# Optimization experiments

Hardware: AMD Instinct MI355X
Metric: run time of the kernel (lower is better)

The kernel has to match this reference:

```python
import jax, jax.numpy as jnp
import numpy as np

B = 16384
D = 1024          # in_features
R = 64            # low_rank
E = 4             # num_experts
L = 3             # layer_num


def setup_inputs() -> dict:
    key = jax.random.key(0)
    ks = jax.random.split(key, 6)
    # xavier-normal-ish scales
    s_uv = (2.0 / (D + R)) ** 0.5
    s_c = (2.0 / (R + R)) ** 0.5
    s_g = (2.0 / (D + 1)) ** 0.5
    return {
        "inputs": jax.random.normal(ks[0], (B, D), dtype=jnp.float32),
        "U": jax.random.normal(ks[1], (L, E, D, R), dtype=jnp.float32) * s_uv,
        "V": jax.random.normal(ks[2], (L, E, D, R), dtype=jnp.float32) * s_uv,
        "C": jax.random.normal(ks[3], (L, E, R, R), dtype=jnp.float32) * s_c,
        "gate_w": jax.random.normal(ks[4], (E, D), dtype=jnp.float32) * s_g,
        "bias": jnp.zeros((L, D), dtype=jnp.float32),
    }


def reference(inputs, U, V, C, gate_w, bias):
    x0 = inputs                                  # [B, D]
    x_l = x0
    for i in range(L):
        # gating: per-expert Linear(d,1) on x_l -> [B, E], softmax over experts
        gates = jax.nn.softmax(x_l @ gate_w.T, axis=1)        # [B, E]
        # v_x = tanh(V_e^T x_l) for all experts at once
        v = jnp.tanh(jnp.einsum('bd,edr->ber', x_l, V[i]))    # [B, E, R]
        v = jnp.tanh(jnp.einsum('ers,bes->ber', C[i], v))     # [B, E, R]
        uv = jnp.einsum('edr,ber->bed', U[i], v)              # [B, E, D]
        dot = x0[:, None, :] * (uv + bias[i][None, None, :])  # [B, E, D]
        moe_out = jnp.einsum('bed,be->bd', dot, gates)        # [B, D]
        x_l = moe_out + x_l
    return x_l
```

## Files before the change

### kernel.cpp

```cpp
#include <hip/hip_runtime.h>
#include <math.h>

#define BB 16384
#define DD 1024
#define RR 64
#define EE 4
#define ER 256
#define LL 3

#define LDM 72

typedef __bf16 bf16x8 __attribute__((ext_vector_type(8)));
typedef float f32x4 __attribute__((ext_vector_type(4)));
typedef unsigned short us;

static __device__ inline us f2b(float f) {
    union { float f; unsigned u; } c; c.f = f;
    return (us)((c.u + 0x7FFF + ((c.u >> 16) & 1)) >> 16);
}
static __device__ inline float b2f(us v) {
    union { unsigned u; float f; } c; c.u = ((unsigned)v) << 16;
    return c.f;
}
static __device__ inline float fast_tanh(float x) {
    float t = __expf(2.f * x);
    return 1.f - 2.f / (t + 1.f);
}
static __device__ __forceinline__ void ld_lds16(const us* g, us* l) {
    __builtin_amdgcn_global_load_lds((const __attribute__((address_space(1))) void*)g,
                                     (__attribute__((address_space(3))) void*)l, 16, 0, 0);
}

__global__ __launch_bounds__(256) void convF2B(const float* __restrict__ s, us* __restrict__ d) {
    int f = (blockIdx.x * 256 + threadIdx.x) * 4;
    float4 v = *(const float4*)&s[f];
    *(ushort4*)&d[f] = make_ushort4(f2b(v.x), f2b(v.y), f2b(v.z), f2b(v.w));
}
__global__ __launch_bounds__(256) void convV(const float* __restrict__ V, us* __restrict__ Vt) {
    const int le = blockIdx.x;
    const int d0 = blockIdx.y * 64;
    __shared__ float t[64 * 65];
    const int tid = threadIdx.x;
    const float* Vb = V + (size_t)le * DD * RR;
    #pragma unroll
    for (int p = 0; p < 4; ++p) {
        int f = tid + p * 256; int dd = f >> 4; int c = (f & 15) * 4;
        float4 v = *(const float4*)&Vb[(size_t)(d0 + dd) * RR + c];
        t[dd * 65 + c + 0] = v.x; t[dd * 65 + c + 1] = v.y;
        t[dd * 65 + c + 2] = v.z; t[dd * 65 + c + 3] = v.w;
    }
    __syncthreads();
    int r = tid >> 2, dg = (tid & 3) * 16;
    us o[16];
    #pragma unroll
    for (int k = 0; k < 16; ++k) o[k] = f2b(t[(dg + k) * 65 + r]);
    us* dst = Vt + (size_t)le * RR * DD + (size_t)r * DD + d0 + dg;
    #pragma unroll
    for (int q = 0; q < 4; ++q) *(ushort4*)&dst[q * 4] = *(ushort4*)&o[q * 4];
}

__global__ __launch_bounds__(512, 2) void layer_fused(const us* __restrict__ xs,
                                                      const us* __restrict__ Vt,
                                                      const us* __restrict__ Ce,
                                                      const us* __restrict__ gwb,
                                                      const us* __restrict__ x0b,
                                                      const us* __restrict__ Ub,
                                                      us* __restrict__ xbo,
                                                      const float* __restrict__ biasl,
                                                      float* __restrict__ out, int last) {
    const int row0 = blockIdx.x * 64;
    const int tid = threadIdx.x;
    const int lane = tid & 63, wave = tid >> 6;
    const int l15 = lane & 15, quad = lane >> 4;
    const int e = wave & 3, h = wave >> 2;
    const int e64 = e * 64;

    __shared__ __align__(16) union {
        struct { us buf[4][10240]; us gw[4096]; float gates[256]; } s;
        us Tt[4][64 * LDM];
        struct { us wlds[64 * 256]; float smf[8][1024]; } p2;
    } u;

    const int kcA  = (lane & 3) ^ ((lane >> 3) & 3);
    const int sA   = quad ^ ((l15 >> 1) & 3);
    const int rsub = lane >> 2;

    ld_lds16(gwb + (size_t)(lane & 3) * DD + (wave * 16 + rsub) * 8, &u.s.gw[wave * 512]);

    auto STAGE = [&](int bi, int k0) {
        us* bb = u.s.buf[bi];
        #pragma unroll
        for (int j = 0; j < 2; ++j) {
            int row = wave * 32 + j * 16 + rsub;
            ld_lds16(Vt + (size_t)row * DD + k0 + kcA * 8, &bb[(wave * 32 + j * 16) * 32]);
        }
        if (wave < 4) {
            int row = wave * 16 + rsub;
            ld_lds16(xs + (size_t)(row0 + row) * DD + k0 + kcA * 8, &bb[8192 + wave * 512]);
        }
    };

    f32x4 acc[4][2] = {};
    f32x4 accg = {};
    STAGE(0, 0); STAGE(1, 32); STAGE(2, 64);

    for (int t = 0; t < 32; ++t) {
        if (t < 30) {
            if (wave < 4) asm volatile("s_waitcnt vmcnt(6)" ::: "memory");
            else          asm volatile("s_waitcnt vmcnt(4)" ::: "memory");
        } else if (t == 30) {
            if (wave < 4) asm volatile("s_waitcnt vmcnt(3)" ::: "memory");
            else          asm volatile("s_waitcnt vmcnt(2)" ::: "memory");
        } else {
            asm volatile("s_waitcnt vmcnt(0)" ::: "memory");
        }
        __builtin_amdgcn_s_barrier();
        if (t < 29) STAGE((t + 3) & 3, (t + 3) * 32);
        __builtin_amdgcn_sched_barrier(0);
        const us* bb = u.s.buf[t & 3];
        bf16x8 af[4], bfr[2];
        #pragma unroll
        for (int mt = 0; mt < 4; ++mt)
            af[mt] = *(const bf16x8*)&bb[(e64 + mt * 16 + l15) * 32 + sA * 8];
        #pragma unroll
        for (int nt = 0; nt < 2; ++nt)
            bfr[nt] = *(const bf16x8*)&bb[8192 + (h * 32 + nt * 16 + l15) * 32 + sA * 8];
        #pragma unroll
        for (int mt = 0; mt < 4; ++mt)
            #pragma unroll
            for (int nt = 0; nt < 2; ++nt)
                acc[mt][nt] = __builtin_amdgcn_mfma_f32_16x16x32_bf16(af[mt], bfr[nt], acc[mt][nt], 0, 0, 0);
        if (wave < 4) {
            bf16x8 bfrg = *(const bf16x8*)&bb[8192 + (wave * 16 + l15) * 32 + sA * 8];
            bf16x8 afg  = *(const bf16x8*)&u.s.gw[(t * 4 + quad) * 32 + (l15 & 3) * 8];
            accg = __builtin_amdgcn_mfma_f32_16x16x32_bf16(afg, bfrg, accg, 0, 0, 0);
        }
    }
    __builtin_amdgcn_s_barrier();
    __builtin_amdgcn_sched_barrier(0);

    {
        us* Tt = u.Tt[e];
        #pragma unroll
        for (int mt = 0; mt < 4; ++mt)
            #pragma unroll
            for (int nt = 0; nt < 2; ++nt) {
                int b = h * 32 + nt * 16 + l15;
                us o[4];
                #pragma unroll
                for (int i = 0; i < 4; ++i) o[i] = f2b(fast_tanh(acc[mt][nt][i]));
                *(ushort4*)&Tt[b * LDM + mt * 16 + quad * 4] = *(ushort4*)o;
            }
    }
    if (wave < 4 && quad == 0) {
        float l0 = accg[0], l1 = accg[1], l2 = accg[2], l3 = accg[3];
        float m = fmaxf(fmaxf(l0, l1), fmaxf(l2, l3));
        float g0 = __expf(l0 - m), g1 = __expf(l1 - m);
        float g2 = __expf(l2 - m), g3 = __expf(l3 - m);
        float inv = 1.f / (g0 + g1 + g2 + g3);
        int b = wave * 16 + l15;
        u.s.gates[0 * 64 + b] = g0 * inv; u.s.gates[1 * 64 + b] = g1 * inv;
        u.s.gates[2 * 64 + b] = g2 * inv; u.s.gates[3 * 64 + b] = g3 * inv;
    }
    __syncthreads();

    const us* Cb = Ce + (size_t)e * RR * RR;
    f32x4 acc2[4][2] = {};
    #pragma unroll
    for (int ks = 0; ks < 2; ++ks) {
        bf16x8 af2[4], bf2[2];
        #pragma unroll
        for (int mt = 0; mt < 4; ++mt)
            af2[mt] = *(const bf16x8*)&Cb[(size_t)(mt * 16 + l15) * RR + ks * 32 + quad * 8];
        #pragma unroll
        for (int nt = 0; nt < 2; ++nt)
            bf2[nt] = *(const bf16x8*)&u.Tt[e][(h * 32 + nt * 16 + l15) * LDM + ks * 32 + quad * 8];
        #pragma unroll
        for (int mt = 0; mt < 4; ++mt)
            #pragma unroll
            for (int nt = 0; nt < 2; ++nt)
                acc2[mt][nt] = __builtin_amdgcn_mfma_f32_16x16x32_bf16(af2[mt], bf2[nt], acc2[mt][nt], 0, 0, 0);
    }
    __syncthreads();

    #pragma unroll
    for (int mt = 0; mt < 4; ++mt)
        #pragma unroll
        for (int nt = 0; nt < 2; ++nt) {
            int b = h * 32 + nt * 16 + l15;
            float g = u.s.gates[e64 + b];
            us o[4];
            #pragma unroll
            for (int i = 0; i < 4; ++i) o[i] = f2b(g * fast_tanh(acc2[mt][nt][i]));
            int col = e64 + mt * 16 + quad * 4;
            int cc = col >> 3, off = col & 7;
            *(ushort4*)&u.p2.wlds[b * 256 + ((cc ^ (b & 7)) << 3) + off] = *(ushort4*)o;
        }
    __syncthreads();

    const int bl = lane >> 2, dc3 = lane & 3;
    #pragma unroll 1
    for (int p = 0; p < 2; ++p) {
        const int dw = p * 512 + wave * 64;
        f32x4 pac[4][4] = {};
        #pragma unroll
        for (int s = 0; s < 8; ++s) {
            int e2 = s >> 1, r0 = (s & 1) * 32;
            bf16x8 af[4], bfr[4];
            #pragma unroll
            for (int mt = 0; mt < 4; ++mt) {
                int d = dw + mt * 16 + l15;
                af[mt] = *(const bf16x8*)&Ub[((size_t)e2 * DD + d) * RR + r0 + quad * 8];
            }
            #pragma unroll
            for (int nt = 0; nt < 4; ++nt) {
                int b = nt * 16 + l15;
                int cc = e2 * 8 + (r0 >> 3) + quad;
                bfr[nt] = *(const bf16x8*)&u.p2.wlds[b * 256 + ((cc ^ (b & 7)) << 3)];
            }
            #pragma unroll
            for (int mt = 0; mt < 4; ++mt)
                #pragma unroll
                for (int nt = 0; nt < 4; ++nt)
                    pac[mt][nt] = __builtin_amdgcn_mfma_f32_16x16x32_bf16(af[mt], bfr[nt], pac[mt][nt], 0, 0, 0);
        }
        const int dg = dw + dc3 * 16;
        float bfv[16];
        *(float4*)&bfv[0]  = *(const float4*)&biasl[dg];
        *(float4*)&bfv[4]  = *(const float4*)&biasl[dg + 4];
        *(float4*)&bfv[8]  = *(const float4*)&biasl[dg + 8];
        *(float4*)&bfv[12] = *(const float4*)&biasl[dg + 12];
        float* smf = u.p2.smf[wave];
        #pragma unroll
        for (int nt = 0; nt < 4; ++nt) {
            #pragma unroll
            for (int mt = 0; mt < 4; ++mt) {
                int ch = (mt * 4 + quad) ^ (l15 & 7);
                *(f32x4*)&smf[l15 * 64 + ch * 4] = pac[mt][nt];
            }
            asm volatile("s_waitcnt lgkmcnt(0)" ::: "memory");
            __builtin_amdgcn_sched_barrier(0);
            const int brow = row0 + nt * 16 + bl;
            const size_t gb = (size_t)brow * DD + dg;
            uint xu[8], lu[8];
            *(uint4*)&xu[0] = *(const uint4*)&x0b[gb];
            *(uint4*)&xu[4] = *(const uint4*)&x0b[gb + 8];
            *(uint4*)&lu[0] = *(const uint4*)&xs[gb];
            *(uint4*)&lu[4] = *(const uint4*)&xs[gb + 8];
            float o[16];
            #pragma unroll
            for (int j = 0; j < 4; ++j) {
                int ch = (dc3 * 4 + j) ^ (bl & 7);
                float4 a = *(const float4*)&smf[bl * 64 + ch * 4];
                #pragma unroll
                for (int i = 0; i < 4; ++i) {
                    int k = j * 4 + i;
                    float av = (i == 0) ? a.x : (i == 1) ? a.y : (i == 2) ? a.z : a.w;
                    uint uu = xu[k >> 1], ll = lu[k >> 1];
                    float xv = b2f((k & 1) ? (us)(uu >> 16) : (us)(uu & 0xffff));
                    float xl = b2f((k & 1) ? (us)(ll >> 16) : (us)(ll & 0xffff));
                    o[k] = xv * (av + bfv[k]) + xl;
                }
            }
            if (last) {
                *(float4*)&out[gb]      = *(float4*)&o[0];
                *(float4*)&out[gb + 4]  = *(float4*)&o[4];
                *(float4*)&out[gb + 8]  = *(float4*)&o[8];
                *(float4*)&out[gb + 12] = *(float4*)&o[12];
            } else {
                us ob[16];
                #pragma unroll
                for (int k = 0; k < 16; ++k) ob[k] = f2b(o[k]);
                *(uint4*)&xbo[gb]     = *(uint4*)&ob[0];
                *(uint4*)&xbo[gb + 8] = *(uint4*)&ob[8];
            }
            asm volatile("s_waitcnt lgkmcnt(0)" ::: "memory");
            __builtin_amdgcn_sched_barrier(0);
        }
    }
}

extern "C" void kernel_launch(void* const* d_in, const int* in_sizes, int n_in,
                              void* d_out, int out_size, void* d_ws, size_t ws_size,
                              hipStream_t stream) {
    const float* inputs = (const float*)d_in[0];
    const float* U      = (const float*)d_in[1];
    const float* V      = (const float*)d_in[2];
    const float* C      = (const float*)d_in[3];
    const float* gw     = (const float*)d_in[4];
    const float* bias   = (const float*)d_in[5];
    float* out = (float*)d_out;

    us* xb0 = (us*)d_ws;
    us* xb  = xb0 + (size_t)BB * DD;
    us* gwb = xb + (size_t)BB * DD;
    us* Vt  = gwb + (size_t)EE * DD;
    us* Ub  = Vt + (size_t)LL * EE * RR * DD;
    us* Cb  = Ub + (size_t)LL * EE * DD * RR;

    convF2B<<<dim3(BB * DD / 1024), 256, 0, stream>>>(inputs, xb0);
    convF2B<<<dim3(LL * EE * DD * RR / 1024), 256, 0, stream>>>(U, Ub);
    convF2B<<<dim3(LL * EE * RR * RR / 1024), 256, 0, stream>>>(C, Cb);
    convF2B<<<dim3(EE * DD / 1024), 256, 0, stream>>>(gw, gwb);
    convV<<<dim3(LL * EE, DD / 64), 256, 0, stream>>>(V, Vt);

    for (int i = 0; i < LL; ++i) {
        const us* xs = (i == 0) ? xb0 : xb;
        layer_fused<<<dim3(BB / 64), 512, 0, stream>>>(
            xs, Vt + (size_t)i * EE * RR * DD, Cb + (size_t)i * EE * RR * RR, gwb,
            xb0, Ub + (size_t)i * EE * DD * RR, xb, bias + (size_t)i * DD,
            out, i == LL - 1);
    }
}
```

Before: 278.7 us.

## Halve row tile to 32 and use triple buffering to raise occupancy

Each block now handles 32 batch rows instead of 64, doubling the grid, and launch bounds ask for 4 blocks per CU instead of 2. The staging pipeline drops from four LDS buffers to three with a prefetch distance of two, and LDS and accumulator sizes shrink to match. The goal is more resident waves to hide memory latency. In exchange, every block still streams the full V and U weight matrices for only half as many rows, so weight traffic and reuse per loaded byte get worse, and the shorter prefetch distance hides less latency per block.

```diff
diff --git a/kernel.cpp b/kernel.cpp
--- a/kernel.cpp
+++ b/kernel.cpp
@@ -59,7 +59,7 @@
     for (int q = 0; q < 4; ++q) *(ushort4*)&dst[q * 4] = *(ushort4*)&o[q * 4];
 }
 
-__global__ __launch_bounds__(512, 2) void layer_fused(const us* __restrict__ xs,
+__global__ __launch_bounds__(512, 4) void layer_fused(const us* __restrict__ xs,
                                                       const us* __restrict__ Vt,
                                                       const us* __restrict__ Ce,
                                                       const us* __restrict__ gwb,
@@ -68,7 +68,7 @@
                                                       us* __restrict__ xbo,
                                                       const float* __restrict__ biasl,
                                                       float* __restrict__ out, int last) {
-    const int row0 = blockIdx.x * 64;
+    const int row0 = blockIdx.x * 32;
     const int tid = threadIdx.x;
     const int lane = tid & 63, wave = tid >> 6;
     const int l15 = lane & 15, quad = lane >> 4;
@@ -76,9 +76,9 @@
     const int e64 = e * 64;
 
     __shared__ __align__(16) union {
-        struct { us buf[4][10240]; us gw[4096]; float gates[256]; } s;
-        us Tt[4][64 * LDM];
-        struct { us wlds[64 * 256]; float smf[8][1024]; } p2;
+        struct { us buf[3][9216]; us gw[4096]; float gates[128]; } s;
+        us Tt[4][32 * LDM];
+        struct { us wlds[32 * 256]; float smf[8][1024]; } p2;
     } u;
 
     const int kcA  = (lane & 3) ^ ((lane >> 3) & 3);
@@ -94,47 +94,45 @@
             int row = wave * 32 + j * 16 + rsub;
             ld_lds16(Vt + (size_t)row * DD + k0 + kcA * 8, &bb[(wave * 32 + j * 16) * 32]);
         }
-        if (wave < 4) {
+        if (wave < 2) {
             int row = wave * 16 + rsub;
             ld_lds16(xs + (size_t)(row0 + row) * DD + k0 + kcA * 8, &bb[8192 + wave * 512]);
         }
     };
 
-    f32x4 acc[4][2] = {};
+    f32x4 acc[4] = {};
     f32x4 accg = {};
-    STAGE(0, 0); STAGE(1, 32); STAGE(2, 64);
-
+    STAGE(0, 0); STAGE(1, 32);
+
+    int cur = 0;
     for (int t = 0; t < 32; ++t) {
-        if (t < 30) {
-            if (wave < 4) asm volatile("s_waitcnt vmcnt(6)" ::: "memory");
-            else          asm volatile("s_waitcnt vmcnt(4)" ::: "memory");
-        } else if (t == 30) {
-            if (wave < 4) asm volatile("s_waitcnt vmcnt(3)" ::: "memory");
+        if (t < 31) {
+            if (wave < 2) asm volatile("s_waitcnt vmcnt(3)" ::: "memory");
             else          asm volatile("s_waitcnt vmcnt(2)" ::: "memory");
         } else {
             asm volatile("s_waitcnt vmcnt(0)" ::: "memory");
         }
         __builtin_amdgcn_s_barrier();
-        if (t < 29) STAGE((t + 3) & 3, (t + 3) * 32);
+        if (t < 30) {
+            int st = cur + 2; if (st >= 3) st -= 3;
+            STAGE(st, (t + 2) * 32);
+        }
         __builtin_amdgcn_sched_barrier(0);
-        const us* bb = u.s.buf[t & 3];
-        bf16x8 af[4], bfr[2];
+        const us* bb = u.s.buf[cur];
+        bf16x8 af[4], bfr;
         #pragma unroll
         for (int mt = 0; mt < 4; ++mt)
             af[mt] = *(const bf16x8*)&bb[(e64 + mt * 16 + l15) * 32 + sA * 8];
-        #pragma unroll
-        for (int nt = 0; nt < 2; ++nt)
-            bfr[nt] = *(const bf16x8*)&bb[8192 + (h * 32 + nt * 16 + l15) * 32 + sA * 8];
+        bfr = *(const bf16x8*)&bb[8192 + (h * 16 + l15) * 32 + sA * 8];
         #pragma unroll
         for (int mt = 0; mt < 4; ++mt)
-            #pragma unroll
-            for (int nt = 0; nt < 2; ++nt)
-                acc[mt][nt] = __builtin_amdgcn_mfma_f32_16x16x32_bf16(af[mt], bfr[nt], acc[mt][nt], 0, 0, 0);
-        if (wave < 4) {
+            acc[mt] = __builtin_amdgcn_mfma_f32_16x16x32_bf16(af[mt], bfr, acc[mt], 0, 0, 0);
+        if (wave < 2) {
             bf16x8 bfrg = *(const bf16x8*)&bb[8192 + (wave * 16 + l15) * 32 + sA * 8];
             bf16x8 afg  = *(const bf16x8*)&u.s.gw[(t * 4 + quad) * 32 + (l15 & 3) * 8];
             accg = __builtin_amdgcn_mfma_f32_16x16x32_bf16(afg, bfrg, accg, 0, 0, 0);
         }
+        cur = (cur + 1 == 3) ? 0 : cur + 1;
     }
     __builtin_amdgcn_s_barrier();
     __builtin_amdgcn_sched_barrier(0);
@@ -142,78 +140,70 @@
     {
         us* Tt = u.Tt[e];
         #pragma unroll
-        for (int mt = 0; mt < 4; ++mt)
-            #pragma unroll
-            for (int nt = 0; nt < 2; ++nt) {
-                int b = h * 32 + nt * 16 + l15;
-                us o[4];
-                #pragma unroll
-                for (int i = 0; i < 4; ++i) o[i] = f2b(fast_tanh(acc[mt][nt][i]));
-                *(ushort4*)&Tt[b * LDM + mt * 16 + quad * 4] = *(ushort4*)o;
-            }
-    }
-    if (wave < 4 && quad == 0) {
+        for (int mt = 0; mt < 4; ++mt) {
+            int b = h * 16 + l15;
+            us o[4];
+            #pragma unroll
+            for (int i = 0; i < 4; ++i) o[i] = f2b(fast_tanh(acc[mt][i]));
+            *(ushort4*)&Tt[b * LDM + mt * 16 + quad * 4] = *(ushort4*)o;
+        }
+    }
+    if (wave < 2 && quad == 0) {
         float l0 = accg[0], l1 = accg[1], l2 = accg[2], l3 = accg[3];
         float m = fmaxf(fmaxf(l0, l1), fmaxf(l2, l3));
         float g0 = __expf(l0 - m), g1 = __expf(l1 - m);
         float g2 = __expf(l2 - m), g3 = __expf(l3 - m);
         float inv = 1.f / (g0 + g1 + g2 + g3);
         int b = wave * 16 + l15;
-        u.s.gates[0 * 64 + b] = g0 * inv; u.s.gates[1 * 64 + b] = g1 * inv;
-        u.s.gates[2 * 64 + b] = g2 * inv; u.s.gates[3 * 64 + b] = g3 * inv;
+        u.s.gates[0 * 32 + b] = g0 * inv; u.s.gates[1 * 32 + b] = g1 * inv;
+        u.s.gates[2 * 32 + b] = g2 * inv; u.s.gates[3 * 32 + b] = g3 * inv;
     }
     __syncthreads();
 
     const us* Cb = Ce + (size_t)e * RR * RR;
-    f32x4 acc2[4][2] = {};
+    f32x4 acc2[4] = {};
     #pragma unroll
     for (int ks = 0; ks < 2; ++ks) {
-        bf16x8 af2[4], bf2[2];
+        bf16x8 af2[4], bf2;
         #pragma unroll
         for (int mt = 0; mt < 4; ++mt)
             af2[mt] = *(const bf16x8*)&Cb[(size_t)(mt * 16 + l15) * RR + ks * 32 + quad * 8];
-        #pragma unroll
-        for (int nt = 0; nt < 2; ++nt)
-            bf2[nt] = *(const bf16x8*)&u.Tt[e][(h * 32 + nt * 16 + l15) * LDM + ks * 32 + quad * 8];
+        bf2 = *(const bf16x8*)&u.Tt[e][(h * 16 + l15) * LDM + ks * 32 + quad * 8];
         #pragma unroll
         for (int mt = 0; mt < 4; ++mt)
-            #pragma unroll
-            for (int nt = 0; nt < 2; ++nt)
-                acc2[mt][nt] = __builtin_amdgcn_mfma_f32_16x16x32_bf16(af2[mt], bf2[nt], acc2[mt][nt], 0, 0, 0);
+            acc2[mt] = __builtin_amdgcn_mfma_f32_16x16x32_bf16(af2[mt], bf2, acc2[mt], 0, 0, 0);
     }
     __syncthreads();
 
     #pragma unroll
-    for (int mt = 0; mt < 4; ++mt)
-        #pragma unroll
-        for (int nt = 0; nt < 2; ++nt) {
-            int b = h * 32 + nt * 16 + l15;
-            float g = u.s.gates[e64 + b];
-            us o[4];
-            #pragma unroll
-            for (int i = 0; i < 4; ++i) o[i] = f2b(g * fast_tanh(acc2[mt][nt][i]));
-            int col = e64 + mt * 16 + quad * 4;
-            int cc = col >> 3, off = col & 7;
-            *(ushort4*)&u.p2.wlds[b * 256 + ((cc ^ (b & 7)) << 3) + off] = *(ushort4*)o;
-        }
+    for (int mt = 0; mt < 4; ++mt) {
+        int b = h * 16 + l15;
+        float g = u.s.gates[e * 32 + b];
+        us o[4];
+        #pragma unroll
+        for (int i = 0; i < 4; ++i) o[i] = f2b(g * fast_tanh(acc2[mt][i]));
+        int col = e64 + mt * 16 + quad * 4;
+        int cc = col >> 3, off = col & 7;
+        *(ushort4*)&u.p2.wlds[b * 256 + ((cc ^ (b & 7)) << 3) + off] = *(ushort4*)o;
+    }
     __syncthreads();
 
     const int bl = lane >> 2, dc3 = lane & 3;
     #pragma unroll 1
     for (int p = 0; p < 2; ++p) {
         const int dw = p * 512 + wave * 64;
-        f32x4 pac[4][4] = {};
+        f32x4 pac[4][2] = {};
         #pragma unroll
         for (int s = 0; s < 8; ++s) {
             int e2 = s >> 1, r0 = (s & 1) * 32;
-            bf16x8 af[4], bfr[4];
+            bf16x8 af[4], bfr[2];
             #pragma unroll
             for (int mt = 0; mt < 4; ++mt) {
                 int d = dw + mt * 16 + l15;
                 af[mt] = *(const bf16x8*)&Ub[((size_t)e2 * DD + d) * RR + r0 + quad * 8];
             }
             #pragma unroll
-            for (int nt = 0; nt < 4; ++nt) {
+            for (int nt = 0; nt < 2; ++nt) {
                 int b = nt * 16 + l15;
                 int cc = e2 * 8 + (r0 >> 3) + quad;
                 bfr[nt] = *(const bf16x8*)&u.p2.wlds[b * 256 + ((cc ^ (b & 7)) << 3)];
@@ -221,7 +211,7 @@
             #pragma unroll
             for (int mt = 0; mt < 4; ++mt)
                 #pragma unroll
-                for (int nt = 0; nt < 4; ++nt)
+                for (int nt = 0; nt < 2; ++nt)
                     pac[mt][nt] = __builtin_amdgcn_mfma_f32_16x16x32_bf16(af[mt], bfr[nt], pac[mt][nt], 0, 0, 0);
         }
         const int dg = dw + dc3 * 16;
@@ -232,7 +222,7 @@
         *(float4*)&bfv[12] = *(const float4*)&biasl[dg + 12];
         float* smf = u.p2.smf[wave];
         #pragma unroll
-        for (int nt = 0; nt < 4; ++nt) {
+        for (int nt = 0; nt < 2; ++nt) {
             #pragma unroll
             for (int mt = 0; mt < 4; ++mt) {
                 int ch = (mt * 4 + quad) ^ (l15 & 7);
@@ -306,7 +296,7 @@
 
     for (int i = 0; i < LL; ++i) {
         const us* xs = (i == 0) ? xb0 : xb;
-        layer_fused<<<dim3(BB / 64), 512, 0, stream>>>(
+        layer_fused<<<dim3(BB / 32), 512, 0, stream>>>(
             xs, Vt + (size_t)i * EE * RR * DD, Cb + (size_t)i * EE * RR * RR, gwb,
             xb0, Ub + (size_t)i * EE * DD * RR, xb, bias + (size_t)i * DD,
             out, i == LL - 1);
```

Result: slower. 329.1 us (+18.1%).

## Replace LDS-staged async pipeline in first GEMM with direct global register loads

Applied to the files above, without the earlier changes.

The first projection GEMM (x·V plus the gate logits) no longer uses a 4-buffer global_load_lds pipeline with explicit vmcnt waits and barriers. Each wave now loads its bf16 fragments straight from global memory into registers inside a fully unrolled loop. The shared-memory union is split into separate arrays, and the barrier after the tanh/gates stage is dropped. This removes per-step barriers and LDS round-trips, but it gives up explicit prefetch overlap and repeats global reads across waves. The larger combined LDS footprint may also stop two blocks from fitting on one CU.

```diff
diff --git a/kernel.cpp b/kernel.cpp
--- a/kernel.cpp
+++ b/kernel.cpp
@@ -25,10 +25,6 @@
 static __device__ inline float fast_tanh(float x) {
     float t = __expf(2.f * x);
     return 1.f - 2.f / (t + 1.f);
-}
-static __device__ __forceinline__ void ld_lds16(const us* g, us* l) {
-    __builtin_amdgcn_global_load_lds((const __attribute__((address_space(1))) void*)g,
-                                     (__attribute__((address_space(3))) void*)l, 16, 0, 0);
 }
 
 __global__ __launch_bounds__(256) void convF2B(const float* __restrict__ s, us* __restrict__ d) {
@@ -75,94 +71,63 @@
     const int e = wave & 3, h = wave >> 2;
     const int e64 = e * 64;
 
-    __shared__ __align__(16) union {
-        struct { us buf[4][10240]; us gw[4096]; float gates[256]; } s;
-        us Tt[4][64 * LDM];
-        struct { us wlds[64 * 256]; float smf[8][1024]; } p2;
-    } u;
-
-    const int kcA  = (lane & 3) ^ ((lane >> 3) & 3);
-    const int sA   = quad ^ ((l15 >> 1) & 3);
-    const int rsub = lane >> 2;
-
-    ld_lds16(gwb + (size_t)(lane & 3) * DD + (wave * 16 + rsub) * 8, &u.s.gw[wave * 512]);
-
-    auto STAGE = [&](int bi, int k0) {
-        us* bb = u.s.buf[bi];
-        #pragma unroll
-        for (int j = 0; j < 2; ++j) {
-            int row = wave * 32 + j * 16 + rsub;
-            ld_lds16(Vt + (size_t)row * DD + k0 + kcA * 8, &bb[(wave * 32 + j * 16) * 32]);
-        }
-        if (wave < 4) {
-            int row = wave * 16 + rsub;
-            ld_lds16(xs + (size_t)(row0 + row) * DD + k0 + kcA * 8, &bb[8192 + wave * 512]);
-        }
-    };
+    __shared__ __align__(16) us    wlds[64 * 256];
+    __shared__ __align__(16) float smf[8][1024];
+    __shared__ __align__(16) us    Tt[4][64 * LDM];
+    __shared__ float gates[256];
+
+    const bool gw4 = (wave < 4);
+
+    const us* vA = Vt + (size_t)(e64 + l15) * DD + quad * 8;
+    const us* xB = xs + (size_t)(row0 + h * 32 + l15) * DD + quad * 8;
+    const us* gA = gwb + (size_t)(l15 & 3) * DD + quad * 8;
+    const us* xG = xs + (size_t)(row0 + (wave & 3) * 16 + l15) * DD + quad * 8;
 
     f32x4 acc[4][2] = {};
     f32x4 accg = {};
-    STAGE(0, 0); STAGE(1, 32); STAGE(2, 64);
-
+
+    #pragma unroll
     for (int t = 0; t < 32; ++t) {
-        if (t < 30) {
-            if (wave < 4) asm volatile("s_waitcnt vmcnt(6)" ::: "memory");
-            else          asm volatile("s_waitcnt vmcnt(4)" ::: "memory");
-        } else if (t == 30) {
-            if (wave < 4) asm volatile("s_waitcnt vmcnt(3)" ::: "memory");
-            else          asm volatile("s_waitcnt vmcnt(2)" ::: "memory");
-        } else {
-            asm volatile("s_waitcnt vmcnt(0)" ::: "memory");
-        }
-        __builtin_amdgcn_s_barrier();
-        if (t < 29) STAGE((t + 3) & 3, (t + 3) * 32);
-        __builtin_amdgcn_sched_barrier(0);
-        const us* bb = u.s.buf[t & 3];
-        bf16x8 af[4], bfr[2];
+        const int kk = t * 32;
+        bf16x8 A[4], B[2];
+        A[0] = *(const bf16x8*)&vA[kk];
+        A[1] = *(const bf16x8*)&vA[16 * DD + kk];
+        A[2] = *(const bf16x8*)&vA[32 * DD + kk];
+        A[3] = *(const bf16x8*)&vA[48 * DD + kk];
+        B[0] = *(const bf16x8*)&xB[kk];
+        B[1] = *(const bf16x8*)&xB[16 * DD + kk];
         #pragma unroll
         for (int mt = 0; mt < 4; ++mt)
-            af[mt] = *(const bf16x8*)&bb[(e64 + mt * 16 + l15) * 32 + sA * 8];
-        #pragma unroll
-        for (int nt = 0; nt < 2; ++nt)
-            bfr[nt] = *(const bf16x8*)&bb[8192 + (h * 32 + nt * 16 + l15) * 32 + sA * 8];
-        #pragma unroll
-        for (int mt = 0; mt < 4; ++mt)
             #pragma unroll
             for (int nt = 0; nt < 2; ++nt)
-                acc[mt][nt] = __builtin_amdgcn_mfma_f32_16x16x32_bf16(af[mt], bfr[nt], acc[mt][nt], 0, 0, 0);
-        if (wave < 4) {
-            bf16x8 bfrg = *(const bf16x8*)&bb[8192 + (wave * 16 + l15) * 32 + sA * 8];
-            bf16x8 afg  = *(const bf16x8*)&u.s.gw[(t * 4 + quad) * 32 + (l15 & 3) * 8];
-            accg = __builtin_amdgcn_mfma_f32_16x16x32_bf16(afg, bfrg, accg, 0, 0, 0);
-        }
-    }
-    __builtin_amdgcn_s_barrier();
-    __builtin_amdgcn_sched_barrier(0);
-
-    {
-        us* Tt = u.Tt[e];
-        #pragma unroll
-        for (int mt = 0; mt < 4; ++mt)
-            #pragma unroll
-            for (int nt = 0; nt < 2; ++nt) {
-                int b = h * 32 + nt * 16 + l15;
-                us o[4];
-                #pragma unroll
-                for (int i = 0; i < 4; ++i) o[i] = f2b(fast_tanh(acc[mt][nt][i]));
-                *(ushort4*)&Tt[b * LDM + mt * 16 + quad * 4] = *(ushort4*)o;
-            }
-    }
-    if (wave < 4 && quad == 0) {
+                acc[mt][nt] = __builtin_amdgcn_mfma_f32_16x16x32_bf16(A[mt], B[nt], acc[mt][nt], 0, 0, 0);
+        if (gw4) {
+            bf16x8 GA = *(const bf16x8*)&gA[kk];
+            bf16x8 GB = *(const bf16x8*)&xG[kk];
+            accg = __builtin_amdgcn_mfma_f32_16x16x32_bf16(GA, GB, accg, 0, 0, 0);
+        }
+    }
+
+    #pragma unroll
+    for (int mt = 0; mt < 4; ++mt)
+        #pragma unroll
+        for (int nt = 0; nt < 2; ++nt) {
+            int b = h * 32 + nt * 16 + l15;
+            us o[4];
+            #pragma unroll
+            for (int i = 0; i < 4; ++i) o[i] = f2b(fast_tanh(acc[mt][nt][i]));
+            *(ushort4*)&Tt[e][b * LDM + mt * 16 + quad * 4] = *(ushort4*)o;
+        }
+    if (gw4 && quad == 0) {
         float l0 = accg[0], l1 = accg[1], l2 = accg[2], l3 = accg[3];
         float m = fmaxf(fmaxf(l0, l1), fmaxf(l2, l3));
         float g0 = __expf(l0 - m), g1 = __expf(l1 - m);
         float g2 = __expf(l2 - m), g3 = __expf(l3 - m);
         float inv = 1.f / (g0 + g1 + g2 + g3);
         int b = wave * 16 + l15;
-        u.s.gates[0 * 64 + b] = g0 * inv; u.s.gates[1 * 64 + b] = g1 * inv;
-        u.s.gates[2 * 64 + b] = g2 * inv; u.s.gates[3 * 64 + b] = g3 * inv;
-    }
-    __syncthreads();
+        gates[0 * 64 + b] = g0 * inv; gates[1 * 64 + b] = g1 * inv;
+        gates[2 * 64 + b] = g2 * inv; gates[3 * 64 + b] = g3 * inv;
+    }
 
     const us* Cb = Ce + (size_t)e * RR * RR;
     f32x4 acc2[4][2] = {};
@@ -174,7 +139,7 @@
             af2[mt] = *(const bf16x8*)&Cb[(size_t)(mt * 16 + l15) * RR + ks * 32 + quad * 8];
         #pragma unroll
         for (int nt = 0; nt < 2; ++nt)
-            bf2[nt] = *(const bf16x8*)&u.Tt[e][(h * 32 + nt * 16 + l15) * LDM + ks * 32 + quad * 8];
+            bf2[nt] = *(const bf16x8*)&Tt[e][(h * 32 + nt * 16 + l15) * LDM + ks * 32 + quad * 8];
         #pragma unroll
         for (int mt = 0; mt < 4; ++mt)
             #pragma unroll
@@ -188,13 +153,13 @@
         #pragma unroll
         for (int nt = 0; nt < 2; ++nt) {
             int b = h * 32 + nt * 16 + l15;
-            float g = u.s.gates[e64 + b];
+            float g = gates[e64 + b];
             us o[4];
             #pragma unroll
             for (int i = 0; i < 4; ++i) o[i] = f2b(g * fast_tanh(acc2[mt][nt][i]));
             int col = e64 + mt * 16 + quad * 4;
             int cc = col >> 3, off = col & 7;
-            *(ushort4*)&u.p2.wlds[b * 256 + ((cc ^ (b & 7)) << 3) + off] = *(ushort4*)o;
+            *(ushort4*)&wlds[b * 256 + ((cc ^ (b & 7)) << 3) + off] = *(ushort4*)o;
         }
     __syncthreads();
 
@@ -216,7 +181,7 @@
             for (int nt = 0; nt < 4; ++nt) {
                 int b = nt * 16 + l15;
                 int cc = e2 * 8 + (r0 >> 3) + quad;
-                bfr[nt] = *(const bf16x8*)&u.p2.wlds[b * 256 + ((cc ^ (b & 7)) << 3)];
+                bfr[nt] = *(const bf16x8*)&wlds[b * 256 + ((cc ^ (b & 7)) << 3)];
             }
             #pragma unroll
             for (int mt = 0; mt < 4; ++mt)
@@ -230,13 +195,13 @@
         *(float4*)&bfv[4]  = *(const float4*)&biasl[dg + 4];
         *(float4*)&bfv[8]  = *(const float4*)&biasl[dg + 8];
         *(float4*)&bfv[12] = *(const float4*)&biasl[dg + 12];
-        float* smf = u.p2.smf[wave];
+        float* sw = smf[wave];
         #pragma unroll
         for (int nt = 0; nt < 4; ++nt) {
             #pragma unroll
             for (int mt = 0; mt < 4; ++mt) {
                 int ch = (mt * 4 + quad) ^ (l15 & 7);
-                *(f32x4*)&smf[l15 * 64 + ch * 4] = pac[mt][nt];
+                *(f32x4*)&sw[l15 * 64 + ch * 4] = pac[mt][nt];
             }
             asm volatile("s_waitcnt lgkmcnt(0)" ::: "memory");
             __builtin_amdgcn_sched_barrier(0);
@@ -251,7 +216,7 @@
             #pragma unroll
             for (int j = 0; j < 4; ++j) {
                 int ch = (dc3 * 4 + j) ^ (bl & 7);
-                float4 a = *(const float4*)&smf[bl * 64 + ch * 4];
+                float4 a = *(const float4*)&sw[bl * 64 + ch * 4];
                 #pragma unroll
                 for (int i = 0; i < 4; ++i) {
                     int k = j * 4 + i;
```

Result: slower. 386.3 us (+38.6%).

## Widen K-tiles to 64 with triple buffering and software-pipeline U loads and epilogue

Applied to the files above, without the earlier changes.

The first GEMM stage now stages 64-wide K tiles in a 3-deep LDS ring instead of 32-wide tiles in a 4-deep ring. This halves the number of barriers and iterations, and the swizzle changes to match the 8-chunk rows. The U-projection loop double-buffers its global U fragment loads so they overlap with MFMAs. The epilogue loads all x0 and x_l tiles up front rather than once per sub-tile. These raise register pressure (launch bounds 512,2) and LDS usage, and one trailing lgkmcnt wait is dropped, which could risk an LDS reuse hazard in the smf scratch.

```diff
diff --git a/kernel.cpp b/kernel.cpp
--- a/kernel.cpp
+++ b/kernel.cpp
@@ -76,83 +76,83 @@
     const int e64 = e * 64;
 
     __shared__ __align__(16) union {
-        struct { us buf[4][10240]; us gw[4096]; float gates[256]; } s;
+        struct { us buf[3][20480]; us gw[4096]; float gates[256]; } s;
         us Tt[4][64 * LDM];
         struct { us wlds[64 * 256]; float smf[8][1024]; } p2;
     } u;
 
-    const int kcA  = (lane & 3) ^ ((lane >> 3) & 3);
-    const int sA   = quad ^ ((l15 >> 1) & 3);
-    const int rsub = lane >> 2;
-
-    ld_lds16(gwb + (size_t)(lane & 3) * DD + (wave * 16 + rsub) * 8, &u.s.gw[wave * 512]);
+    const bool gw4 = (wave < 4);
+    const int r8   = lane >> 3;
+    const int cA8  = (lane & 7) ^ r8;
+    const int l7   = l15 & 7;
+
+    ld_lds16(gwb + (size_t)(lane & 3) * DD + (wave * 16 + (lane >> 2)) * 8, &u.s.gw[wave * 512]);
 
     auto STAGE = [&](int bi, int k0) {
         us* bb = u.s.buf[bi];
         #pragma unroll
-        for (int j = 0; j < 2; ++j) {
-            int row = wave * 32 + j * 16 + rsub;
-            ld_lds16(Vt + (size_t)row * DD + k0 + kcA * 8, &bb[(wave * 32 + j * 16) * 32]);
-        }
-        if (wave < 4) {
-            int row = wave * 16 + rsub;
-            ld_lds16(xs + (size_t)(row0 + row) * DD + k0 + kcA * 8, &bb[8192 + wave * 512]);
+        for (int j = 0; j < 4; ++j) {
+            int row = wave * 32 + j * 8 + r8;
+            ld_lds16(Vt + (size_t)row * DD + k0 + cA8 * 8, &bb[(wave * 256 + j * 64) * 8]);
+        }
+        {
+            int row = wave * 8 + r8;
+            ld_lds16(xs + (size_t)(row0 + row) * DD + k0 + cA8 * 8, &bb[16384 + wave * 512]);
         }
     };
 
     f32x4 acc[4][2] = {};
     f32x4 accg = {};
-    STAGE(0, 0); STAGE(1, 32); STAGE(2, 64);
-
-    for (int t = 0; t < 32; ++t) {
-        if (t < 30) {
-            if (wave < 4) asm volatile("s_waitcnt vmcnt(6)" ::: "memory");
-            else          asm volatile("s_waitcnt vmcnt(4)" ::: "memory");
-        } else if (t == 30) {
-            if (wave < 4) asm volatile("s_waitcnt vmcnt(3)" ::: "memory");
-            else          asm volatile("s_waitcnt vmcnt(2)" ::: "memory");
-        } else {
-            asm volatile("s_waitcnt vmcnt(0)" ::: "memory");
-        }
+    STAGE(0, 0); STAGE(1, 64);
+
+    int cur = 0;
+    for (int t = 0; t < 16; ++t) {
+        if (t < 15) asm volatile("s_waitcnt vmcnt(5)" ::: "memory");
+        else        asm volatile("s_waitcnt vmcnt(0)" ::: "memory");
         __builtin_amdgcn_s_barrier();
-        if (t < 29) STAGE((t + 3) & 3, (t + 3) * 32);
+        if (t < 14) {
+            int st = cur + 2; if (st >= 3) st -= 3;
+            STAGE(st, (t + 2) * 64);
+        }
         __builtin_amdgcn_sched_barrier(0);
-        const us* bb = u.s.buf[t & 3];
-        bf16x8 af[4], bfr[2];
-        #pragma unroll
-        for (int mt = 0; mt < 4; ++mt)
-            af[mt] = *(const bf16x8*)&bb[(e64 + mt * 16 + l15) * 32 + sA * 8];
-        #pragma unroll
-        for (int nt = 0; nt < 2; ++nt)
-            bfr[nt] = *(const bf16x8*)&bb[8192 + (h * 32 + nt * 16 + l15) * 32 + sA * 8];
-        #pragma unroll
-        for (int mt = 0; mt < 4; ++mt)
+        const us* bb = u.s.buf[cur];
+        #pragma unroll
+        for (int ks = 0; ks < 2; ++ks) {
+            const int sl = ((ks * 4 + quad) ^ l7) * 8;
+            bf16x8 af[4], bfr[2];
+            #pragma unroll
+            for (int mt = 0; mt < 4; ++mt)
+                af[mt] = *(const bf16x8*)&bb[(e64 + mt * 16 + l15) * 64 + sl];
             #pragma unroll
             for (int nt = 0; nt < 2; ++nt)
-                acc[mt][nt] = __builtin_amdgcn_mfma_f32_16x16x32_bf16(af[mt], bfr[nt], acc[mt][nt], 0, 0, 0);
-        if (wave < 4) {
-            bf16x8 bfrg = *(const bf16x8*)&bb[8192 + (wave * 16 + l15) * 32 + sA * 8];
-            bf16x8 afg  = *(const bf16x8*)&u.s.gw[(t * 4 + quad) * 32 + (l15 & 3) * 8];
-            accg = __builtin_amdgcn_mfma_f32_16x16x32_bf16(afg, bfrg, accg, 0, 0, 0);
-        }
+                bfr[nt] = *(const bf16x8*)&bb[16384 + (h * 32 + nt * 16 + l15) * 64 + sl];
+            #pragma unroll
+            for (int mt = 0; mt < 4; ++mt)
+                #pragma unroll
+                for (int nt = 0; nt < 2; ++nt)
+                    acc[mt][nt] = __builtin_amdgcn_mfma_f32_16x16x32_bf16(af[mt], bfr[nt], acc[mt][nt], 0, 0, 0);
+            if (gw4) {
+                bf16x8 bfrg = *(const bf16x8*)&bb[16384 + (wave * 16 + l15) * 64 + sl];
+                bf16x8 afg  = *(const bf16x8*)&u.s.gw[((t * 8 + ks * 4 + quad) * 4 + (l15 & 3)) * 8];
+                accg = __builtin_amdgcn_mfma_f32_16x16x32_bf16(afg, bfrg, accg, 0, 0, 0);
+            }
+        }
+        cur = (cur == 2) ? 0 : cur + 1;
     }
     __builtin_amdgcn_s_barrier();
     __builtin_amdgcn_sched_barrier(0);
 
-    {
-        us* Tt = u.Tt[e];
-        #pragma unroll
-        for (int mt = 0; mt < 4; ++mt)
-            #pragma unroll
-            for (int nt = 0; nt < 2; ++nt) {
-                int b = h * 32 + nt * 16 + l15;
-                us o[4];
-                #pragma unroll
-                for (int i = 0; i < 4; ++i) o[i] = f2b(fast_tanh(acc[mt][nt][i]));
-                *(ushort4*)&Tt[b * LDM + mt * 16 + quad * 4] = *(ushort4*)o;
-            }
-    }
-    if (wave < 4 && quad == 0) {
+    #pragma unroll
+    for (int mt = 0; mt < 4; ++mt)
+        #pragma unroll
+        for (int nt = 0; nt < 2; ++nt) {
+            int b = h * 32 + nt * 16 + l15;
+            us o[4];
+            #pragma unroll
+            for (int i = 0; i < 4; ++i) o[i] = f2b(fast_tanh(acc[mt][nt][i]));
+            *(ushort4*)&u.Tt[e][b * LDM + mt * 16 + quad * 4] = *(ushort4*)o;
+        }
+    if (gw4 && quad == 0) {
         float l0 = accg[0], l1 = accg[1], l2 = accg[2], l3 = accg[3];
         float m = fmaxf(fmaxf(l0, l1), fmaxf(l2, l3));
         float g0 = __expf(l0 - m), g1 = __expf(l1 - m);
@@ -203,55 +203,71 @@
     for (int p = 0; p < 2; ++p) {
         const int dw = p * 512 + wave * 64;
         f32x4 pac[4][4] = {};
-        #pragma unroll
-        for (int s = 0; s < 8; ++s) {
-            int e2 = s >> 1, r0 = (s & 1) * 32;
-            bf16x8 af[4], bfr[4];
-            #pragma unroll
-            for (int mt = 0; mt < 4; ++mt) {
-                int d = dw + mt * 16 + l15;
-                af[mt] = *(const bf16x8*)&Ub[((size_t)e2 * DD + d) * RR + r0 + quad * 8];
-            }
-            #pragma unroll
-            for (int nt = 0; nt < 4; ++nt) {
-                int b = nt * 16 + l15;
-                int cc = e2 * 8 + (r0 >> 3) + quad;
-                bfr[nt] = *(const bf16x8*)&u.p2.wlds[b * 256 + ((cc ^ (b & 7)) << 3)];
-            }
-            #pragma unroll
-            for (int mt = 0; mt < 4; ++mt)
-                #pragma unroll
-                for (int nt = 0; nt < 4; ++nt)
-                    pac[mt][nt] = __builtin_amdgcn_mfma_f32_16x16x32_bf16(af[mt], bfr[nt], pac[mt][nt], 0, 0, 0);
-        }
+        bf16x8 a0[4], a1[4];
+        #define LOADU(dst, S) { const int e2 = (S) >> 1, r0q = ((S) & 1) * 32;            \
+            _Pragma("unroll")                                                              \
+            for (int mt = 0; mt < 4; ++mt) {                                               \
+                int d = dw + mt * 16 + l15;                                                \
+                dst[mt] = *(const bf16x8*)&Ub[((size_t)e2 * DD + d) * RR + r0q + quad * 8];\
+            } }
+        #define LOADW(dst, S) { const int e2 = (S) >> 1, r0q = ((S) & 1) * 32;            \
+            _Pragma("unroll")                                                              \
+            for (int nt = 0; nt < 4; ++nt) {                                               \
+                int b = nt * 16 + l15;                                                     \
+                int cc = e2 * 8 + (r0q >> 3) + quad;                                       \
+                dst[nt] = *(const bf16x8*)&u.p2.wlds[b * 256 + ((cc ^ (b & 7)) << 3)];     \
+            } }
+        #define MM(A, W) { _Pragma("unroll")                                               \
+            for (int mt = 0; mt < 4; ++mt) { _Pragma("unroll")                             \
+                for (int nt = 0; nt < 4; ++nt)                                             \
+                    pac[mt][nt] = __builtin_amdgcn_mfma_f32_16x16x32_bf16(A[mt], W[nt], pac[mt][nt], 0, 0, 0); } }
+        LOADU(a0, 0);
+        #pragma unroll
+        for (int sp = 0; sp < 4; ++sp) {
+            bf16x8 w0[4], w1[4];
+            LOADU(a1, 2 * sp + 1);
+            LOADW(w0, 2 * sp);
+            MM(a0, w0);
+            if (sp < 3) LOADU(a0, 2 * sp + 2);
+            LOADW(w1, 2 * sp + 1);
+            MM(a1, w1);
+        }
+        #undef LOADU
+        #undef LOADW
+        #undef MM
+
         const int dg = dw + dc3 * 16;
+        uint4 X[4][2], L[4][2];
+        #pragma unroll
+        for (int nt = 0; nt < 4; ++nt) {
+            const size_t gb = (size_t)(row0 + nt * 16 + bl) * DD + dg;
+            X[nt][0] = *(const uint4*)&x0b[gb];     X[nt][1] = *(const uint4*)&x0b[gb + 8];
+            L[nt][0] = *(const uint4*)&xs[gb];      L[nt][1] = *(const uint4*)&xs[gb + 8];
+        }
         float bfv[16];
         *(float4*)&bfv[0]  = *(const float4*)&biasl[dg];
         *(float4*)&bfv[4]  = *(const float4*)&biasl[dg + 4];
         *(float4*)&bfv[8]  = *(const float4*)&biasl[dg + 8];
         *(float4*)&bfv[12] = *(const float4*)&biasl[dg + 12];
-        float* smf = u.p2.smf[wave];
+        float* sw = u.p2.smf[wave];
         #pragma unroll
         for (int nt = 0; nt < 4; ++nt) {
             #pragma unroll
             for (int mt = 0; mt < 4; ++mt) {
                 int ch = (mt * 4 + quad) ^ (l15 & 7);
-                *(f32x4*)&smf[l15 * 64 + ch * 4] = pac[mt][nt];
+                *(f32x4*)&sw[l15 * 64 + ch * 4] = pac[mt][nt];
             }
             asm volatile("s_waitcnt lgkmcnt(0)" ::: "memory");
             __builtin_amdgcn_sched_barrier(0);
-            const int brow = row0 + nt * 16 + bl;
-            const size_t gb = (size_t)brow * DD + dg;
+            const size_t gb = (size_t)(row0 + nt * 16 + bl) * DD + dg;
             uint xu[8], lu[8];
-            *(uint4*)&xu[0] = *(const uint4*)&x0b[gb];
-            *(uint4*)&xu[4] = *(const uint4*)&x0b[gb + 8];
-            *(uint4*)&lu[0] = *(const uint4*)&xs[gb];
-            *(uint4*)&lu[4] = *(const uint4*)&xs[gb + 8];
+            *(uint4*)&xu[0] = X[nt][0]; *(uint4*)&xu[4] = X[nt][1];
+            *(uint4*)&lu[0] = L[nt][0]; *(uint4*)&lu[4] = L[nt][1];
             float o[16];
             #pragma unroll
             for (int j = 0; j < 4; ++j) {
                 int ch = (dc3 * 4 + j) ^ (bl & 7);
-                float4 a = *(const float4*)&smf[bl * 64 + ch * 4];
+                float4 a = *(const float4*)&sw[bl * 64 + ch * 4];
                 #pragma unroll
                 for (int i = 0; i < 4; ++i) {
                     int k = j * 4 + i;
@@ -274,8 +290,6 @@
                 *(uint4*)&xbo[gb]     = *(uint4*)&ob[0];
                 *(uint4*)&xbo[gb + 8] = *(uint4*)&ob[8];
             }
-            asm volatile("s_waitcnt lgkmcnt(0)" ::: "memory");
-            __builtin_amdgcn_sched_barrier(0);
         }
     }
 }
```

Measured after the change: 276.5 us. About the same (-0.8%).
